# Kernel tuning notes

Measured on AMD Instinct MI355X. Metric: run time of the kernel, lower is better.

The kernel has to match this reference:

```python
import jax, jax.numpy as jnp
import numpy as np

B, N, L, D = 64, 512, 12, 128   # batch, nodes, neighbors, node_dim==edge_dim
Z = 3 * D                        # 2*node_dim + edge_dim
NC = 3                           # n_convs
VOCAB = 1000
BN_EPS = 1e-3                    # keras BatchNormalization default epsilon


def setup_inputs() -> dict:
    key = jax.random.key(0)
    ks = jax.random.split(key, 14)
    inp = {}
    inp['node_types'] = jax.random.randint(ks[0], (B, N), 0, VOCAB)
    inp['neighbor_list'] = jax.random.randint(ks[1], (B, N, L), 0, N)
    inp['edge_types'] = jax.random.randint(ks[2], (B, N, L), 0, VOCAB)
    inp['slot_types'] = jax.random.normal(ks[3], (B, N, D), jnp.float32)
    inp['node_w'] = jax.random.normal(ks[4], (VOCAB, D), jnp.float32) * 0.1
    inp['edge_w'] = jax.random.normal(ks[5], (VOCAB, D), jnp.float32) * 0.1
    inp['wf'] = jax.random.normal(ks[6], (NC, Z, D), jnp.float32) * 0.05
    inp['bf'] = jax.random.normal(ks[7], (NC, D), jnp.float32) * 0.01
    inp['ws'] = jax.random.normal(ks[8], (NC, Z, D), jnp.float32) * 0.05
    inp['bs'] = jax.random.normal(ks[9], (NC, D), jnp.float32) * 0.01
    inp['bn_gamma'] = jnp.ones((NC, D), jnp.float32)
    inp['bn_beta'] = jnp.zeros((NC, D), jnp.float32)
    inp['bn_mean'] = jax.random.normal(ks[10], (NC, D), jnp.float32) * 0.01
    inp['bn_var'] = jax.random.uniform(ks[11], (NC, D), jnp.float32, 0.5, 1.5)
    inp['dense_w'] = jax.random.normal(ks[12], (D, 1), jnp.float32) * 0.1
    inp['dense_b'] = jnp.zeros((1,), jnp.float32)
    return inp


def _embed(w, x):
    # gather with negative-index masking, as in Embedding.call (inference path)
    idx = jnp.where(x < 0, 0, x)
    mask = (x >= 0).astype(jnp.float32)[..., None]
    return w[idx] * mask


def reference(node_types, neighbor_list, edge_types, slot_types,
              node_w, edge_w, wf, bf, ws, bs,
              bn_gamma, bn_beta, bn_mean, bn_var, dense_w, dense_b):
    v = _embed(node_w, node_types) + slot_types          # (B, N, D)
    e = _embed(edge_w, edge_types)                       # (B, N, L, D)

    nl = neighbor_list
    n_safe = jnp.where(nl < 0, 0, nl)                    # (B, N, L)
    nmask = (nl >= 0).astype(jnp.float32)[..., None]     # (B, N, L, 1)

    for i in range(NC):
        # neighbor gather: per-batch index into node axis
        nn = jax.vmap(lambda vv, ii: vv[ii])(v, n_safe) * nmask  # (B, N, L, D)
        v_view = jnp.broadcast_to(v[:, :, None, :], nn.shape)
        z = jnp.concatenate([v_view, nn, e], axis=-1)            # (B, N, L, Z)
        s = (jax.nn.sigmoid(jnp.einsum('bnlz,zd->bnld', z, wf[i]) + bf[i])
             * jnp.tanh(jnp.einsum('bnlz,zd->bnld', z, ws[i]) + bs[i])
             * nmask)
        v_next = v + jnp.sum(s, axis=2)                          # (B, N, D)

        # masked batchnorm (inference: moving stats); invalid rows -> 0
        vf = v_next.reshape(-1, D)
        valid = jnp.all(jnp.abs(vf) > 1e-5, axis=-1)
        bn = bn_gamma[i] * (vf - bn_mean[i]) * jax.lax.rsqrt(bn_var[i] + BN_EPS) + bn_beta[i]
        v = jnp.where(valid[:, None], bn, 0.0).reshape(B, N, D)

    # masked mean pooling over nodes
    pmask = (node_types >= 0).astype(jnp.float32)[..., None]     # (B, N, 1)
    pooled = jnp.sum(v * pmask, axis=1) / jnp.sum(pmask, axis=1)  # (B, D)
    return pooled @ dense_w + dense_b                            # (B, 1)
```

## Files before the change

kernel.cpp:

```cpp
#include <hip/hip_runtime.h>

#define NB 64
#define NN 512
#define NL 12
#define ND 128
#define NZ 384
#define NCONV 3
#define VOCAB 1000
#define BN_EPS 1e-3f
#define LO_SCALE 2048.0f
#define INV_LO (1.0f/2048.0f)
#define SCF (-1.4426950408889634f)
#define SCS ( 2.8853900817779268f)

typedef _Float16 f16;
using half8 = __attribute__((ext_vector_type(8))) _Float16;
using floatx16 = __attribute__((ext_vector_type(16))) float;

__device__ __forceinline__ floatx16 mfma32(half8 a, half8 b, floatx16 c) {
    return __builtin_amdgcn_mfma_f32_32x32x16_f16(a, b, c, 0, 0, 0);
}
__device__ __forceinline__ void split1(float x, f16& h, f16& l) {
    h = (f16)x; l = (f16)((x - (float)h) * LO_SCALE);
}
__device__ __forceinline__ float4 gload4(const float* addr) {
    float4 r;
    asm volatile("global_load_dwordx4 %0, %1, off"
                 : "=&v"(r) : "v"(addr));
    return r;
}

__global__ __launch_bounds__(256) void setup_kernel(
    const float* __restrict__ wf, const float* __restrict__ wsg,
    f16* __restrict__ Wc_hi, f16* __restrict__ Wc_lo,
    const float* __restrict__ edge_w, float* __restrict__ EWp,
    const float* __restrict__ bn_gamma, const float* __restrict__ bn_beta,
    const float* __restrict__ bn_mean, const float* __restrict__ bn_var,
    float* __restrict__ bnp,
    const int* __restrict__ node_types, const float* __restrict__ slot_types,
    const float* __restrict__ node_w, float* __restrict__ vA)
{
    __shared__ float se[32][128];
    const int blk = blockIdx.x;
    const int tid = threadIdx.x;
    if (blk < 768) {
        int id = blk * 256 + tid;
        int c = id >> 16;
        int rem = id & 65535;
        int col = rem >> 7, k = rem & 127;
        int part = col >> 7;
        int d = col & 127;
        int z = (part < 2) ? (128 + k) : k;
        const float* W = (part & 1) ? wsg : wf;
        float wv = W[((size_t)c * NZ + z) * ND + d];
        f16 h, l; split1(wv, h, l);
        size_t dst = (size_t)c * 65536 + (size_t)(k >> 3) * 4096 + col * 8 + (k & 7);
        Wc_hi[dst] = h; Wc_lo[dst] = l;
    } else if (blk < 864) {
        const int bid = blk - 768;
        const int c = bid >> 5;
        const int tyg = (bid & 31) * 32;
        for (int i = tid; i < 4096; i += 256) {
            int ty = i >> 7, k = i & 127;
            int tyv = tyg + ty;
            se[ty][k] = (tyv < VOCAB) ? edge_w[(size_t)tyv * ND + k] : 0.f;
        }
        __syncthreads();
        const int h = tid >> 7, col = tid & 127;
        const float* W = h ? wsg : wf;
        const float sc = h ? SCS : SCF;
        float acc[32];
        #pragma unroll
        for (int ty = 0; ty < 32; ++ty) acc[ty] = 0.f;
        #pragma unroll 4
        for (int k = 0; k < 128; ++k) {
            float wv = W[((size_t)c * NZ + 256 + k) * ND + col];
            #pragma unroll
            for (int ty = 0; ty < 32; ++ty) acc[ty] = fmaf(se[ty][k], wv, acc[ty]);
        }
        #pragma unroll
        for (int ty = 0; ty < 32; ++ty) {
            int tyv = tyg + ty;
            if (tyv <= VOCAB)
                EWp[((size_t)c * (VOCAB + 1) + tyv) * 256 + (col & 63) * 4 + (col >> 6) * 2 + h] = acc[ty] * sc;
        }
    } else if (blk < 866) {
        int t = (blk - 864) * 256 + tid;
        if (t < NCONV * ND) {
            int c = t >> 7, j = t & 127;
            float4 q;
            q.x = bn_gamma[c * ND + j];
            q.y = bn_beta[c * ND + j];
            q.z = bn_mean[c * ND + j];
            q.w = 1.f / sqrtf(bn_var[c * ND + j] + BN_EPS);
            *(float4*)(bnp + (size_t)t * 4) = q;
        }
    } else {
        int i = (blk - 866) * 256 + tid;
        int bn = i >> 7, d = i & 127;
        int ty = node_types[bn];
        float m = ty >= 0 ? 1.f : 0.f;
        int idx = ty >= 0 ? ty : 0;
        vA[i] = node_w[(size_t)idx * ND + d] * m + slot_types[i];
    }
}

__global__ __launch_bounds__(256, 3) void psgemm_kernel(
    const float* __restrict__ vA,
    const f16* __restrict__ Wc_hi, const f16* __restrict__ Wc_lo,
    const float* __restrict__ bfv, const float* __restrict__ bsv,
    float* __restrict__ Ppk, float* __restrict__ Spk)
{
    __shared__ __align__(16) char sA[16384];
    const int hw = blockIdx.x;
    const int xcd = hw & 7;
    const int q = hw >> 3;
    const int bl = q >> 5;
    const int r = q & 31;
    const int half = r >> 4;
    const int xloc = r & 15;
    const int batch = bl * 8 + xcd;
    const int node0 = batch * NN + xloc * 32;

    const int tid = threadIdx.x;
    const int lane = tid & 63, w = tid >> 6;
    const int l31 = lane & 31, l32 = lane >> 5;

    #pragma unroll
    for (int it = 0; it < 2; ++it) {
        int slot = it * 256 + tid;
        int rr = slot >> 4, cc = slot & 15;
        int cs = cc ^ (rr & 15);
        const float* vp = vA + (size_t)(node0 + rr) * ND + cs * 8;
        float4 u0 = *(const float4*)vp;
        float4 u1 = *(const float4*)(vp + 4);
        float uu[8] = {u0.x, u0.y, u0.z, u0.w, u1.x, u1.y, u1.z, u1.w};
        half8 hh, ll;
        #pragma unroll
        for (int jj = 0; jj < 8; ++jj) {
            f16 h, l; split1(uu[jj], h, l);
            hh[jj] = h; ll[jj] = l;
        }
        *(half8*)(sA + rr * 256 + cc * 16) = hh;
        *(half8*)(sA + 8192 + rr * 256 + cc * 16) = ll;
    }
    __syncthreads();

    const int dcol = w * 32 + l31;
    const int col0 = half * 256 + dcol;
    const int col1 = col0 + 128;

    floatx16 a00 = {}, a10 = {}, a01 = {}, a11 = {};

    half8 B[3][4];
    #define LDB(dst, ks) { \
        size_t k0 = (size_t)((ks) * 2 + l32) * 4096; \
        (dst)[0] = *(const half8*)(Wc_hi + k0 + col0 * 8); \
        (dst)[1] = *(const half8*)(Wc_lo + k0 + col0 * 8); \
        (dst)[2] = *(const half8*)(Wc_hi + k0 + col1 * 8); \
        (dst)[3] = *(const half8*)(Wc_lo + k0 + col1 * 8); }
    LDB(B[0], 0)
    LDB(B[1], 1)

    #pragma unroll
    for (int ks = 0; ks < 8; ++ks) {
        if (ks < 6) LDB(B[(ks + 2) % 3], ks + 2)
        const half8* Bc = B[ks % 3];
        int qq = (((ks * 2 + l32) ^ (l31 & 15)) << 4);
        half8 ah = *(const half8*)(sA + l31 * 256 + qq);
        half8 al = *(const half8*)(sA + 8192 + l31 * 256 + qq);
        a00 = mfma32(ah, Bc[0], a00);
        a10 = mfma32(ah, Bc[1], a10);
        a10 = mfma32(al, Bc[0], a10);
        a01 = mfma32(ah, Bc[2], a01);
        a11 = mfma32(ah, Bc[3], a11);
        a11 = mfma32(al, Bc[2], a11);
    }
    #undef LDB

    float bx = 0.f, by = 0.f;
    if (half) { bx = bfv[dcol]; by = bsv[dcol]; }
    float* outp = half ? Spk : Ppk;
    const int dsub = (dcol & 63) * 4 + (dcol >> 6) * 2;
    #pragma unroll
    for (int rr = 0; rr < 16; ++rr) {
        int orow = (rr & 3) + 8 * (rr >> 2) + 4 * l32;
        float2 v2 = { (a00[rr] + a10[rr] * INV_LO + bx) * SCF,
                      (a01[rr] + a11[rr] * INV_LO + by) * SCS };
        *(float2*)(outp + (size_t)(node0 + orow) * 256 + dsub) = v2;
    }
}

__global__ __launch_bounds__(256, 4) void edge_epilogue_kernel(
    float* __restrict__ vA,
    const int* __restrict__ neighbor_list, const int* __restrict__ edge_types,
    const float* __restrict__ Ppk, const float* __restrict__ Spk,
    const float* __restrict__ EWp, const float* __restrict__ bnp)
{
    __shared__ float s_red[2][64][2];
    const int hw = blockIdx.x;
    const int xcd = hw & 7;
    const int q = hw >> 3;
    const int b = (q >> 8) * 8 + xcd;
    const int j = q & 255;
    const int node0 = b * NN + j * 2;

    const int tid = threadIdx.x;
    const int w = tid >> 6, ds = tid & 63;
    const int nl_ = w >> 1;
    const int sub = w & 1;
    const int node = node0 + nl_;
    const int bbase = b * NN;

    int nlv = -1, etv = -1;
    if (ds < 6) {
        nlv = neighbor_list[node * NL + sub * 6 + ds];
        etv = edge_types[node * NL + sub * 6 + ds];
    }
    unsigned long long bm = __ballot(nlv >= 0);

    float4 sp4 = gload4(Spk + (size_t)node * 256 + ds * 4);
    float4 p4[6], e4[6];
    #pragma unroll
    for (int l = 0; l < 6; ++l) {
        int nl_l = __builtin_amdgcn_readlane(nlv, l);
        int ns = (nl_l >= 0) ? (bbase + nl_l) : node;
        p4[l] = gload4(Ppk + (size_t)ns * 256 + ds * 4);
    }
    #pragma unroll
    for (int l = 0; l < 6; ++l) {
        int et_l = __builtin_amdgcn_readlane(etv, l);
        int es = (et_l >= 0) ? et_l : VOCAB;
        e4[l] = gload4(EWp + (size_t)es * 256 + ds * 4);
    }
    asm volatile("s_waitcnt vmcnt(0)" ::: "memory");
    __builtin_amdgcn_sched_barrier(0);

    float sum0 = 0.f, sum1 = 0.f;
    #pragma unroll
    for (int l = 0; l < 6; ++l) {
        float m = ((bm >> l) & 1) ? 1.f : 0.f;
        float ax = p4[l].x + sp4.x + e4[l].x;
        float ay = p4[l].y + sp4.y + e4[l].y;
        float az = p4[l].z + sp4.z + e4[l].z;
        float aw = p4[l].w + sp4.w + e4[l].w;
        float u0 = __builtin_amdgcn_exp2f(fminf(ax, 60.f));
        float w0 = __builtin_amdgcn_exp2f(fminf(ay, 60.f));
        float u1 = __builtin_amdgcn_exp2f(fminf(az, 60.f));
        float w1 = __builtin_amdgcn_exp2f(fminf(aw, 60.f));
        float r0 = __builtin_amdgcn_rcpf(fmaf(u0, w0, 1.f + u0 + w0));
        float r1 = __builtin_amdgcn_rcpf(fmaf(u1, w1, 1.f + u1 + w1));
        sum0 = fmaf((w0 - 1.f) * r0, m, sum0);
        sum1 = fmaf((w1 - 1.f) * r1, m, sum1);
    }

    if (sub) { s_red[nl_][ds][0] = sum0; s_red[nl_][ds][1] = sum1; }
    __syncthreads();
    if (!sub) {
        sum0 += s_red[nl_][ds][0];
        sum1 += s_red[nl_][ds][1];
        size_t i0 = (size_t)node * ND + ds;
        size_t i1 = i0 + 64;
        float x0 = vA[i0] + sum0;
        float x1 = vA[i1] + sum1;
        int valid = __all(fabsf(x0) > 1e-5f && fabsf(x1) > 1e-5f);
        float4 q0 = *(const float4*)(bnp + (size_t)ds * 4);
        float4 q1 = *(const float4*)(bnp + (size_t)(ds + 64) * 4);
        vA[i0] = valid ? (q0.x * (x0 - q0.z) * q0.w + q0.y) : 0.f;
        vA[i1] = valid ? (q1.x * (x1 - q1.z) * q1.w + q1.y) : 0.f;
    }
}

__global__ __launch_bounds__(512) void pool_kernel(
    const float* __restrict__ vA, const int* __restrict__ node_types,
    const float* __restrict__ dense_w, const float* __restrict__ dense_b,
    float* __restrict__ out)
{
    __shared__ float s_sum[4][128];
    __shared__ float s_cnt[4];
    __shared__ float s_part[2];
    const int b = blockIdx.x;
    const int tid = threadIdx.x;
    const int d = tid & 127, chunk = tid >> 7;
    const int nbase = b * NN + chunk * 128;
    float sum = 0.f, cnt = 0.f;
    #pragma unroll 4
    for (int i = 0; i < 128; ++i) {
        int ty = node_types[nbase + i];
        float mk = ty >= 0 ? 1.f : 0.f;
        sum += vA[(size_t)(nbase + i) * ND + d] * mk;
        cnt += mk;
    }
    s_sum[chunk][d] = sum;
    if (d == 0) s_cnt[chunk] = cnt;
    __syncthreads();
    if (chunk == 0) {
        float tot = s_sum[0][d] + s_sum[1][d] + s_sum[2][d] + s_sum[3][d];
        float tcnt = s_cnt[0] + s_cnt[1] + s_cnt[2] + s_cnt[3];
        float pv = (tot / tcnt) * dense_w[d];
        #pragma unroll
        for (int off = 32; off > 0; off >>= 1) pv += __shfl_down(pv, off);
        if ((d & 63) == 0) s_part[d >> 6] = pv;
    }
    __syncthreads();
    if (tid == 0) out[b] = s_part[0] + s_part[1] + dense_b[0];
}

extern "C" void kernel_launch(void* const* d_in, const int* in_sizes, int n_in,
                              void* d_out, int out_size, void* d_ws, size_t ws_size,
                              hipStream_t stream) {
    const int*   node_types    = (const int*)d_in[0];
    const int*   neighbor_list = (const int*)d_in[1];
    const int*   edge_types    = (const int*)d_in[2];
    const float* slot_types    = (const float*)d_in[3];
    const float* node_w        = (const float*)d_in[4];
    const float* edge_w        = (const float*)d_in[5];
    const float* wf            = (const float*)d_in[6];
    const float* bfv           = (const float*)d_in[7];
    const float* wsg           = (const float*)d_in[8];
    const float* bsv           = (const float*)d_in[9];
    const float* bn_gamma      = (const float*)d_in[10];
    const float* bn_beta       = (const float*)d_in[11];
    const float* bn_mean       = (const float*)d_in[12];
    const float* bn_var        = (const float*)d_in[13];
    const float* dense_w       = (const float*)d_in[14];
    const float* dense_b       = (const float*)d_in[15];
    float* out = (float*)d_out;

    float* wsf = (float*)d_ws;
    float* Ppk = wsf;
    float* Spk = wsf + 8388608;
    float* EWp = wsf + 2 * 8388608;
    float* bnp = EWp + 768768;
    float* vA  = bnp + 1536;
    f16* Wc_hi = (f16*)(vA + 4194304);
    f16* Wc_lo = Wc_hi + 196608;

    setup_kernel<<<17250, 256, 0, stream>>>(
        wf, wsg, Wc_hi, Wc_lo, edge_w, EWp,
        bn_gamma, bn_beta, bn_mean, bn_var, bnp,
        node_types, slot_types, node_w, vA);

    for (int c = 0; c < NCONV; ++c) {
        psgemm_kernel<<<2048, 256, 0, stream>>>(
            vA, Wc_hi + (size_t)c * 65536, Wc_lo + (size_t)c * 65536,
            bfv + c * ND, bsv + c * ND, Ppk, Spk);
        edge_epilogue_kernel<<<16384, 256, 0, stream>>>(
            vA, neighbor_list, edge_types,
            Ppk, Spk, EWp + (size_t)c * (VOCAB + 1) * 256,
            bnp + (size_t)c * 512);
    }

    pool_kernel<<<NB, 512, 0, stream>>>(vA, node_types, dense_w, dense_b, out);
}
```

Measured before the change: 256.6 us.

## Stage edge-epilogue gathers through LDS with direct global-to-LDS loads

```diff
diff --git a/kernel.cpp b/kernel.cpp
--- a/kernel.cpp
+++ b/kernel.cpp
@@ -23,11 +23,10 @@
 __device__ __forceinline__ void split1(float x, f16& h, f16& l) {
     h = (f16)x; l = (f16)((x - (float)h) * LO_SCALE);
 }
-__device__ __forceinline__ float4 gload4(const float* addr) {
-    float4 r;
-    asm volatile("global_load_dwordx4 %0, %1, off"
-                 : "=&v"(r) : "v"(addr));
-    return r;
+__device__ __forceinline__ void gl_lds16(const void* g, void* l) {
+    __builtin_amdgcn_global_load_lds(
+        (const __attribute__((address_space(1))) void*)g,
+        (__attribute__((address_space(3))) void*)l, 16, 0, 0);
 }
 
 __global__ __launch_bounds__(256) void setup_kernel(
@@ -191,12 +190,13 @@
     }
 }
 
-__global__ __launch_bounds__(256, 4) void edge_epilogue_kernel(
+__global__ __launch_bounds__(256, 3) void edge_epilogue_kernel(
     float* __restrict__ vA,
     const int* __restrict__ neighbor_list, const int* __restrict__ edge_types,
     const float* __restrict__ Ppk, const float* __restrict__ Spk,
     const float* __restrict__ EWp, const float* __restrict__ bnp)
 {
+    __shared__ __align__(16) char sL[2][25600];
     __shared__ float s_red[2][64][2];
     const int hw = blockIdx.x;
     const int xcd = hw & 7;
@@ -206,44 +206,63 @@
     const int node0 = b * NN + j * 2;
 
     const int tid = threadIdx.x;
-    const int w = tid >> 6, ds = tid & 63;
+    const int w = tid >> 6, lane = tid & 63;
     const int nl_ = w >> 1;
-    const int sub = w & 1;
+    const int part = w & 1;
     const int node = node0 + nl_;
     const int bbase = b * NN;
 
     int nlv = -1, etv = -1;
-    if (ds < 6) {
-        nlv = neighbor_list[node * NL + sub * 6 + ds];
-        etv = edge_types[node * NL + sub * 6 + ds];
+    if (lane < NL) {
+        nlv = neighbor_list[node * NL + lane];
+        etv = edge_types[node * NL + lane];
     }
     unsigned long long bm = __ballot(nlv >= 0);
 
-    float4 sp4 = gload4(Spk + (size_t)node * 256 + ds * 4);
-    float4 p4[6], e4[6];
-    #pragma unroll
-    for (int l = 0; l < 6; ++l) {
-        int nl_l = __builtin_amdgcn_readlane(nlv, l);
-        int ns = (nl_l >= 0) ? (bbase + nl_l) : node;
-        p4[l] = gload4(Ppk + (size_t)ns * 256 + ds * 4);
-    }
-    #pragma unroll
-    for (int l = 0; l < 6; ++l) {
-        int et_l = __builtin_amdgcn_readlane(etv, l);
-        int es = (et_l >= 0) ? et_l : VOCAB;
-        e4[l] = gload4(EWp + (size_t)es * 256 + ds * 4);
-    }
-    asm volatile("s_waitcnt vmcnt(0)" ::: "memory");
-    __builtin_amdgcn_sched_barrier(0);
-
+    char* nb = sL[nl_];
+    if (!part) {
+        gl_lds16(Spk + (size_t)node * 256 + lane * 4, nb);
+        #pragma unroll
+        for (int l = 0; l < 9; ++l) {
+            int nlx = __builtin_amdgcn_readlane(nlv, l);
+            int ns = (nlx >= 0) ? (bbase + nlx) : node;
+            gl_lds16(Ppk + (size_t)ns * 256 + lane * 4, nb + 1024 + l * 1024);
+        }
+        #pragma unroll
+        for (int e = 9; e < 12; ++e) {
+            int et = __builtin_amdgcn_readlane(etv, e);
+            int es = (et >= 0) ? et : VOCAB;
+            gl_lds16(EWp + (size_t)es * 256 + lane * 4, nb + 13312 + e * 1024);
+        }
+    } else {
+        #pragma unroll
+        for (int l = 9; l < 12; ++l) {
+            int nlx = __builtin_amdgcn_readlane(nlv, l);
+            int ns = (nlx >= 0) ? (bbase + nlx) : node;
+            gl_lds16(Ppk + (size_t)ns * 256 + lane * 4, nb + 1024 + l * 1024);
+        }
+        #pragma unroll
+        for (int e = 0; e < 9; ++e) {
+            int et = __builtin_amdgcn_readlane(etv, e);
+            int es = (et >= 0) ? et : VOCAB;
+            gl_lds16(EWp + (size_t)es * 256 + lane * 4, nb + 13312 + e * 1024);
+        }
+    }
+    __syncthreads();
+
+    const int ds = lane;
+    float4 sp4 = *(const float4*)(nb + ds * 16);
     float sum0 = 0.f, sum1 = 0.f;
     #pragma unroll
     for (int l = 0; l < 6; ++l) {
-        float m = ((bm >> l) & 1) ? 1.f : 0.f;
-        float ax = p4[l].x + sp4.x + e4[l].x;
-        float ay = p4[l].y + sp4.y + e4[l].y;
-        float az = p4[l].z + sp4.z + e4[l].z;
-        float aw = p4[l].w + sp4.w + e4[l].w;
+        int e = part * 6 + l;
+        float m = ((bm >> e) & 1) ? 1.f : 0.f;
+        float4 p4 = *(const float4*)(nb + 1024 + e * 1024 + ds * 16);
+        float4 e4 = *(const float4*)(nb + 13312 + e * 1024 + ds * 16);
+        float ax = p4.x + sp4.x + e4.x;
+        float ay = p4.y + sp4.y + e4.y;
+        float az = p4.z + sp4.z + e4.z;
+        float aw = p4.w + sp4.w + e4.w;
         float u0 = __builtin_amdgcn_exp2f(fminf(ax, 60.f));
         float w0 = __builtin_amdgcn_exp2f(fminf(ay, 60.f));
         float u1 = __builtin_amdgcn_exp2f(fminf(az, 60.f));
@@ -254,9 +273,9 @@
         sum1 = fmaf((w1 - 1.f) * r1, m, sum1);
     }
 
-    if (sub) { s_red[nl_][ds][0] = sum0; s_red[nl_][ds][1] = sum1; }
-    __syncthreads();
-    if (!sub) {
+    if (part) { s_red[nl_][ds][0] = sum0; s_red[nl_][ds][1] = sum1; }
+    __syncthreads();
+    if (!part) {
         sum0 += s_red[nl_][ds][0];
         sum1 += s_red[nl_][ds][1];
         size_t i0 = (size_t)node * ND + ds;
```

After: 340.0 us. 1.32x slower.
